# Optimization experiments

Measured on AMD Instinct MI355X. Metric: run time of the kernel, lower is better.

The kernel has to match this reference:

```python
import jax, jax.numpy as jnp
import numpy as np

HEAD_DIM = 64
HIDDEN_SIZE = 3072
NUM_HEADS = 48
B, TXT, VID = 1, 256, 1792
N = TXT + VID


def _layernorm(x, g, b, eps=1e-5):
    mu = jnp.mean(x, axis=-1, keepdims=True)
    xc = x - mu
    var = jnp.mean(xc * xc, axis=-1, keepdims=True)
    return xc * jax.lax.rsqrt(var + eps) * g + b


def _apply_rope1(x, freqs):
    # x: [B, L, H, D]; freqs: [1, 1, Lf, D//2, 2, 2]
    Bx, L, H, D = x.shape
    x_ = x.reshape(Bx, L, H, D // 2, 1, 2)
    # faithful to torch: if dim-2 sizes mismatch (H vs Lf), slice freqs to H
    if x_.shape[2] != 1 and freqs.shape[2] != 1 and x_.shape[2] != freqs.shape[2]:
        freqs = freqs[:, :, : x_.shape[2]]
    out = freqs[..., 0] * x_[..., 0] + freqs[..., 1] * x_[..., 1]
    return out.reshape(Bx, L, H, D).astype(x.dtype)


def setup_inputs() -> dict:
    key = jax.random.key(0)
    ks = jax.random.split(key, 16)
    s = 1.0 / np.sqrt(HIDDEN_SIZE)
    d = dict(
        combined=jax.random.normal(ks[0], (B, N, HIDDEN_SIZE), jnp.float32),
        freqs=jax.random.normal(ks[1], (1, 1, VID, HEAD_DIM // 2, 2, 2), jnp.float32),
        Wq=jax.random.normal(ks[2], (HIDDEN_SIZE, HIDDEN_SIZE), jnp.float32) * s,
        bq=jnp.zeros((HIDDEN_SIZE,), jnp.float32),
        Wk=jax.random.normal(ks[3], (HIDDEN_SIZE, HIDDEN_SIZE), jnp.float32) * s,
        bk=jnp.zeros((HIDDEN_SIZE,), jnp.float32),
        Wv=jax.random.normal(ks[4], (HIDDEN_SIZE, HIDDEN_SIZE), jnp.float32) * s,
        bv=jnp.zeros((HIDDEN_SIZE,), jnp.float32),
        Wo=jax.random.normal(ks[5], (HIDDEN_SIZE, HIDDEN_SIZE), jnp.float32) * s,
        bo=jnp.zeros((HIDDEN_SIZE,), jnp.float32),
        gq=jnp.ones((HEAD_DIM,), jnp.float32),
        bgq=jnp.zeros((HEAD_DIM,), jnp.float32),
        gk=jnp.ones((HEAD_DIM,), jnp.float32),
        bgk=jnp.zeros((HEAD_DIM,), jnp.float32),
        txt_len=TXT,
    )
    return d


def reference(combined, freqs, Wq, bq, Wk, bk, Wv, bv, Wo, bo, gq, bgq, gk, bgk, txt_len):
    Bx, Nx, _ = combined.shape
    Q = (combined @ Wq.T + bq).reshape(Bx, Nx, NUM_HEADS, HEAD_DIM)
    K = (combined @ Wk.T + bk).reshape(Bx, Nx, NUM_HEADS, HEAD_DIM)
    V = (combined @ Wv.T + bv).reshape(Bx, Nx, NUM_HEADS, HEAD_DIM)
    Q = _layernorm(Q, gq, bgq)
    K = _layernorm(K, gk, bgk)
    if freqs is not None and Nx - txt_len > 0:
        Q_vid = _apply_rope1(Q[:, txt_len:], freqs)
        K_vid = _apply_rope1(K[:, txt_len:], freqs)
        Q = jnp.concatenate([Q[:, :txt_len], Q_vid], axis=1)
        K = jnp.concatenate([K[:, :txt_len], K_vid], axis=1)
    # SDPA in fp32: [B, H, N, D]
    q = Q.transpose(0, 2, 1, 3).astype(jnp.float32)
    k = K.transpose(0, 2, 1, 3).astype(jnp.float32)
    v = V.transpose(0, 2, 1, 3).astype(jnp.float32)
    scale = 1.0 / np.sqrt(HEAD_DIM)
    scores = jnp.einsum('bhqd,bhkd->bhqk', q, k) * scale
    probs = jax.nn.softmax(scores, axis=-1)
    attn = jnp.einsum('bhqk,bhkd->bhqd', probs, v).astype(combined.dtype)
    attn = attn.transpose(0, 2, 1, 3).reshape(Bx, Nx, HIDDEN_SIZE)
    out = attn @ Wo.T + bo
    return out[:, txt_len:], out[:, :txt_len]
```

## Files before the change

### kernel.cpp

```cpp
#include <hip/hip_runtime.h>
#include <hip/hip_bf16.h>

typedef __attribute__((ext_vector_type(8))) short bf16x8;
typedef __attribute__((ext_vector_type(4))) float f32x4;
typedef unsigned int __attribute__((address_space(1))) as1_uint;
typedef unsigned int __attribute__((address_space(3))) as3_uint;

#define TXT 256
#define VIDN 1792
#define SEQ 2048
#define HID 3072
#define NH 48
#define HD 64
#define QSCALE 0.18033688011112042f

__device__ __forceinline__ unsigned short f2bf(float f) {
  union { float f; unsigned int u; } x; x.f = f;
  unsigned int r = x.u + 0x7fffu + ((x.u >> 16) & 1u);
  return (unsigned short)(r >> 16);
}

__device__ __forceinline__ void gload16(const void* g, void* l) {
  __builtin_amdgcn_global_load_lds((const as1_uint*)g, (as3_uint*)l, 16, 0, 0);
}

__device__ __forceinline__ void fbar() {
  asm volatile("" ::: "memory");
  __builtin_amdgcn_s_barrier();
  asm volatile("" ::: "memory");
}

__global__ __launch_bounds__(256) void cvt_kernel(const float* __restrict__ s,
                                                  unsigned short* __restrict__ d, int n) {
  int i = (blockIdx.x * 256 + threadIdx.x) * 4;
  if (i >= n) return;
  float4 v = *(const float4*)(s + i);
  ushort4 o;
  o.x = f2bf(v.x); o.y = f2bf(v.y); o.z = f2bf(v.z); o.w = f2bf(v.w);
  *(ushort4*)(d + i) = o;
}

__global__ __launch_bounds__(256) void cvt3_kernel(const float* __restrict__ a,
                                                   const float* __restrict__ b,
                                                   const float* __restrict__ c,
                                                   unsigned short* __restrict__ d) {
  const int per = (HID * HID) / 1024;
  int bid = blockIdx.x;
  int m = bid / per, r = bid - m * per;
  const float* s = (m == 0) ? a : (m == 1) ? b : c;
  int i = (r * 256 + threadIdx.x) * 4;
  float4 v = *(const float4*)(s + i);
  ushort4 o;
  o.x = f2bf(v.x); o.y = f2bf(v.y); o.z = f2bf(v.z); o.w = f2bf(v.w);
  *(ushort4*)(d + (size_t)m * HID * HID + i) = o;
}

template<int MODE>
__global__ __launch_bounds__(512, 4) void gemm256(
    const unsigned short* __restrict__ A,
    const unsigned short* __restrict__ Bt,
    int K, int ntn,
    float* __restrict__ Cq, unsigned short* __restrict__ Vt, const float* __restrict__ bv,
    float* __restrict__ Cout, const float* __restrict__ bo)
{
  __shared__ unsigned short lds[3 * 8192];
  const int tid = threadIdx.x;
  const int mt = blockIdx.x / ntn, nt = blockIdx.x % ntn;
  const int m0 = mt * 128, n0 = nt * 128;
  const int w = tid >> 6, lane = tid & 63, lr = lane & 15, lg = lane >> 4;
  const int wr = w >> 2, wc = w & 3;
  f32x4 acc[4][2] = {};
  const int NT = K >> 5;

  const int soff  = tid * 16;
  const int soffs = soff ^ (((soff >> 7) & 3) << 4);
  const int srow  = soffs >> 6;
  const int scol  = (soffs & 63) >> 1;
  const unsigned short* Asrc = A + (size_t)(m0 + srow) * K + scol;
  const unsigned short* Bsrc = Bt + (size_t)(n0 + srow) * K + scol;

  int aoff[4], boff[2];
#pragma unroll
  for (int mf = 0; mf < 4; ++mf) {
    int arow = wr * 64 + mf * 16 + lr;
    aoff[mf] = arow * 32 + (lg ^ ((arow >> 1) & 3)) * 8;
  }
#pragma unroll
  for (int nf = 0; nf < 2; ++nf) {
    int brow = wc * 32 + nf * 16 + lr;
    boff[nf] = brow * 32 + (lg ^ ((brow >> 1) & 3)) * 8;
  }

#define STAGE(t)                                                               \
  {                                                                            \
    const int slot_ = (t) % 3;                                                 \
    const int k0_ = (t) << 5;                                                  \
    char* base_ = (char*)lds + slot_ * 16384;                                  \
    gload16(Asrc + k0_, base_ + soff);                                         \
    gload16(Bsrc + k0_, base_ + 8192 + soff);                                  \
  }

#define COMPUTE(t)                                                             \
  {                                                                            \
    const unsigned short* lA = lds + ((t) % 3) * 8192;                         \
    const unsigned short* lB = lA + 4096;                                      \
    bf16x8 bfr[2];                                                             \
    _Pragma("unroll")                                                          \
    for (int nf = 0; nf < 2; ++nf)                                             \
      bfr[nf] = *(const bf16x8*)&lB[boff[nf]];                                 \
    __builtin_amdgcn_s_setprio(1);                                             \
    _Pragma("unroll")                                                          \
    for (int mf = 0; mf < 4; ++mf) {                                           \
      bf16x8 af = *(const bf16x8*)&lA[aoff[mf]];                               \
      acc[mf][0] = __builtin_amdgcn_mfma_f32_16x16x32_bf16(af, bfr[0], acc[mf][0], 0, 0, 0); \
      acc[mf][1] = __builtin_amdgcn_mfma_f32_16x16x32_bf16(af, bfr[1], acc[mf][1], 0, 0, 0); \
    }                                                                          \
    __builtin_amdgcn_s_setprio(0);                                             \
  }

  STAGE(0); STAGE(1);
  int t = 0;
  for (; t < NT - 2; ++t) {
    STAGE(t + 2);
    asm volatile("s_waitcnt vmcnt(4)" ::: "memory");
    fbar();
    COMPUTE(t);
    fbar();
  }
  asm volatile("s_waitcnt vmcnt(2)" ::: "memory");
  fbar();
  COMPUTE(t); ++t;
  fbar();
  asm volatile("s_waitcnt vmcnt(0)" ::: "memory");
  fbar();
  COMPUTE(t);
#undef STAGE
#undef COMPUTE

  if (MODE == 0) {
    if (n0 < 6144) {
#pragma unroll
      for (int mf = 0; mf < 4; ++mf) {
        int row = m0 + wr * 64 + mf * 16 + lg * 4;
#pragma unroll
        for (int nf = 0; nf < 2; ++nf) {
          int col = n0 + wc * 32 + nf * 16 + lr;
#pragma unroll
          for (int j = 0; j < 4; ++j)
            Cq[(size_t)(row + j) * 6144 + col] = acc[mf][nf][j];
        }
      }
    } else {
#pragma unroll
      for (int mf = 0; mf < 4; ++mf) {
        int srow2 = m0 + wr * 64 + mf * 16 + lg * 4;
#pragma unroll
        for (int nf = 0; nf < 2; ++nf) {
          int n2 = n0 - 6144 + wc * 32 + nf * 16 + lr;
          float b = bv[n2];
          ushort4 pk;
          pk.x = f2bf(acc[mf][nf][0] + b);
          pk.y = f2bf(acc[mf][nf][1] + b);
          pk.z = f2bf(acc[mf][nf][2] + b);
          pk.w = f2bf(acc[mf][nf][3] + b);
          *(ushort4*)(Vt + (size_t)n2 * SEQ + srow2) = pk;
        }
      }
    }
  } else {
#pragma unroll
    for (int mf = 0; mf < 4; ++mf) {
      int row = m0 + wr * 64 + mf * 16 + lg * 4;
#pragma unroll
      for (int nf = 0; nf < 2; ++nf) {
        int col = n0 + wc * 32 + nf * 16 + lr;
        float b = bo[col];
#pragma unroll
        for (int j = 0; j < 4; ++j) {
          int s = row + j;
          int orow = (s >= TXT) ? (s - TXT) : (VIDN + s);
          Cout[(size_t)orow * HID + col] = acc[mf][nf][j] + b;
        }
      }
    }
  }
}

__global__ __launch_bounds__(256) void ln_rope_kernel(
    const float* __restrict__ QK,
    const float* __restrict__ bq, const float* __restrict__ bk,
    const float* __restrict__ gq, const float* __restrict__ bgq,
    const float* __restrict__ gk, const float* __restrict__ bgk,
    const float* __restrict__ freqs,
    unsigned short* __restrict__ Qh, unsigned short* __restrict__ Kh)
{
  int wid = blockIdx.x * 4 + (threadIdx.x >> 6);
  int lane = threadIdx.x & 63;
  int s = wid / 96;
  int rem = wid - s * 96;
  int h = rem >> 1, qk = rem & 1;
  int col = h * 64 + lane;
  float x = QK[(size_t)s * 6144 + qk * 3072 + col] + (qk ? bk[col] : bq[col]);
  float m = x;
#pragma unroll
  for (int msk = 1; msk < 64; msk <<= 1) m += __shfl_xor(m, msk);
  float mu = m * (1.0f / 64.0f);
  float xc = x - mu;
  float v = xc * xc;
#pragma unroll
  for (int msk = 1; msk < 64; msk <<= 1) v += __shfl_xor(v, msk);
  float rstd = rsqrtf(v * (1.0f / 64.0f) + 1e-5f);
  float y = xc * rstd * (qk ? gk[lane] : gq[lane]) + (qk ? bgk[lane] : bgq[lane]);
  if (s >= TXT) {
    float p = __shfl_xor(y, 1);
    float xe = (lane & 1) ? p : y;
    float xo = (lane & 1) ? y : p;
    int base = h * 128 + (lane >> 1) * 4 + (lane & 1) * 2;
    y = freqs[base] * xe + freqs[base + 1] * xo;
  }
  if (!qk) y *= QSCALE;
  (qk ? Kh : Qh)[((size_t)h * SEQ + s) * 64 + lane] = f2bf(y);
}

__global__ __launch_bounds__(512) void fattn_kernel(
    const unsigned short* __restrict__ Qh, const unsigned short* __restrict__ Kh,
    const unsigned short* __restrict__ Vt, unsigned short* __restrict__ ctx)
{
  __shared__ unsigned short kt[2][64][32];
  __shared__ unsigned short vt[2][64][32];
  __shared__ unsigned short pl[8][16][72];
  const int h = blockIdx.x >> 4;
  const int q0 = (blockIdx.x & 15) * 128;
  const int tid = threadIdx.x, w = tid >> 6, lane = tid & 63, lr = lane & 15, lg = lane >> 4;

  bf16x8 qf0, qf1;
  {
    const unsigned short* qp = Qh + ((size_t)h * SEQ + q0 + w * 16 + lr) * 64 + lg * 8;
    qf0 = *(const bf16x8*)qp;
    qf1 = *(const bf16x8*)(qp + 32);
  }
  f32x4 oacc[4] = {};
  float mrun = -1e30f, lrun = 0.f;

  for (int kv0 = 0; kv0 < SEQ; kv0 += 64) {
    __syncthreads();
    {
      int off = tid * 16;
      int half = off >> 12;
      int rem = off & 4095;
      int row = rem >> 6, cb = rem & 63;
      gload16(Kh + ((size_t)h * SEQ + kv0 + row) * 64 + half * 32 + (cb >> 1), (char*)kt + off);
      gload16(Vt + ((size_t)(h * 64 + row)) * SEQ + kv0 + half * 32 + (cb >> 1), (char*)vt + off);
    }
    __syncthreads();

    f32x4 sacc[4] = {};
    __builtin_amdgcn_s_setprio(1);
#pragma unroll
    for (int nf = 0; nf < 4; ++nf) {
      bf16x8 a0 = *(const bf16x8*)&kt[0][nf * 16 + lr][lg * 8];
      bf16x8 a1 = *(const bf16x8*)&kt[1][nf * 16 + lr][lg * 8];
      sacc[nf] = __builtin_amdgcn_mfma_f32_16x16x32_bf16(a0, qf0, sacc[nf], 0, 0, 0);
      sacc[nf] = __builtin_amdgcn_mfma_f32_16x16x32_bf16(a1, qf1, sacc[nf], 0, 0, 0);
    }
    __builtin_amdgcn_s_setprio(0);

    float mx;
    {
      float t0 = fmaxf(fmaxf(sacc[0][0], sacc[0][1]), fmaxf(sacc[0][2], sacc[0][3]));
      float t1 = fmaxf(fmaxf(sacc[1][0], sacc[1][1]), fmaxf(sacc[1][2], sacc[1][3]));
      float t2 = fmaxf(fmaxf(sacc[2][0], sacc[2][1]), fmaxf(sacc[2][2], sacc[2][3]));
      float t3 = fmaxf(fmaxf(sacc[3][0], sacc[3][1]), fmaxf(sacc[3][2], sacc[3][3]));
      mx = fmaxf(fmaxf(t0, t1), fmaxf(t2, t3));
    }
    mx = fmaxf(mx, __shfl_xor(mx, 16));
    mx = fmaxf(mx, __shfl_xor(mx, 32));

    if (!__all(mx <= mrun + 8.0f)) {
      float mn = fmaxf(mrun, mx);
      float corr = exp2f(mrun - mn);
      lrun *= corr;
      mrun = mn;
      float c0 = __shfl(corr, lg * 4 + 0);
      float c1 = __shfl(corr, lg * 4 + 1);
      float c2 = __shfl(corr, lg * 4 + 2);
      float c3 = __shfl(corr, lg * 4 + 3);
#pragma unroll
      for (int df = 0; df < 4; ++df) {
        oacc[df][0] *= c0; oacc[df][1] *= c1;
        oacc[df][2] *= c2; oacc[df][3] *= c3;
      }
    }

    float pr[4][4];
#pragma unroll
    for (int nf = 0; nf < 4; ++nf)
#pragma unroll
      for (int r = 0; r < 4; ++r)
        pr[nf][r] = exp2f(sacc[nf][r] - mrun);
    float rs;
    {
      float s0 = (pr[0][0] + pr[0][1]) + (pr[0][2] + pr[0][3]);
      float s1 = (pr[1][0] + pr[1][1]) + (pr[1][2] + pr[1][3]);
      float s2 = (pr[2][0] + pr[2][1]) + (pr[2][2] + pr[2][3]);
      float s3 = (pr[3][0] + pr[3][1]) + (pr[3][2] + pr[3][3]);
      rs = (s0 + s1) + (s2 + s3);
    }
    rs += __shfl_xor(rs, 16);
    rs += __shfl_xor(rs, 32);
    lrun += rs;

#pragma unroll
    for (int nf = 0; nf < 4; ++nf) {
      union { __hip_bfloat162 h; unsigned int u; } c0, c1;
      c0.h = __float22bfloat162_rn(make_float2(pr[nf][0], pr[nf][1]));
      c1.h = __float22bfloat162_rn(make_float2(pr[nf][2], pr[nf][3]));
      uint2 pw; pw.x = c0.u; pw.y = c1.u;
      *(uint2*)&pl[w][lr][nf * 16 + lg * 4] = pw;
    }

    bf16x8 pa0 = *(const bf16x8*)&pl[w][lr][lg * 8];
    bf16x8 pa1 = *(const bf16x8*)&pl[w][lr][32 + lg * 8];
    __builtin_amdgcn_s_setprio(1);
#pragma unroll
    for (int df = 0; df < 4; ++df) {
      bf16x8 v0 = *(const bf16x8*)&vt[0][df * 16 + lr][lg * 8];
      bf16x8 v1 = *(const bf16x8*)&vt[1][df * 16 + lr][lg * 8];
      oacc[df] = __builtin_amdgcn_mfma_f32_16x16x32_bf16(pa0, v0, oacc[df], 0, 0, 0);
      oacc[df] = __builtin_amdgcn_mfma_f32_16x16x32_bf16(pa1, v1, oacc[df], 0, 0, 0);
    }
    __builtin_amdgcn_s_setprio(0);
  }

  float linv = 1.0f / lrun;
  float i0 = __shfl(linv, lg * 4 + 0);
  float i1 = __shfl(linv, lg * 4 + 1);
  float i2 = __shfl(linv, lg * 4 + 2);
  float i3 = __shfl(linv, lg * 4 + 3);
#pragma unroll
  for (int df = 0; df < 4; ++df) {
    int s = q0 + w * 16 + lg * 4;
    int dcol = h * 64 + df * 16 + lr;
    ctx[(size_t)(s + 0) * HID + dcol] = f2bf(oacc[df][0] * i0);
    ctx[(size_t)(s + 1) * HID + dcol] = f2bf(oacc[df][1] * i1);
    ctx[(size_t)(s + 2) * HID + dcol] = f2bf(oacc[df][2] * i2);
    ctx[(size_t)(s + 3) * HID + dcol] = f2bf(oacc[df][3] * i3);
  }
}

extern "C" void kernel_launch(void* const* d_in, const int* in_sizes, int n_in,
                              void* d_out, int out_size, void* d_ws, size_t ws_size,
                              hipStream_t stream) {
  const float* combined = (const float*)d_in[0];
  const float* freqs    = (const float*)d_in[1];
  const float* Wq  = (const float*)d_in[2];
  const float* bq  = (const float*)d_in[3];
  const float* Wk  = (const float*)d_in[4];
  const float* bk  = (const float*)d_in[5];
  const float* Wv  = (const float*)d_in[6];
  const float* bv  = (const float*)d_in[7];
  const float* Wo  = (const float*)d_in[8];
  const float* bo  = (const float*)d_in[9];
  const float* gq  = (const float*)d_in[10];
  const float* bgq = (const float*)d_in[11];
  const float* gk  = (const float*)d_in[12];
  const float* bgk = (const float*)d_in[13];
  float* out = (float*)d_out;

  char* ws = (char*)d_ws;
  unsigned short* Abf  = (unsigned short*)ws; ws += (size_t)SEQ * HID * 2;
  unsigned short* Wqkv = (unsigned short*)ws; ws += (size_t)3 * HID * HID * 2;
  float*          QK   = (float*)ws;          ws += (size_t)SEQ * 6144 * 4;
  unsigned short* Qh   = (unsigned short*)ws; ws += (size_t)NH * SEQ * HD * 2;
  unsigned short* Kh   = (unsigned short*)ws; ws += (size_t)NH * SEQ * HD * 2;
  unsigned short* Vt   = (unsigned short*)ws; ws += (size_t)NH * HD * SEQ * 2;
  unsigned short* Wob  = (unsigned short*)QK;
  unsigned short* ctx  = Abf;

  cvt_kernel<<<(SEQ * HID) / 1024, 256, 0, stream>>>(combined, Abf, SEQ * HID);
  cvt3_kernel<<<3 * (HID * HID) / 1024, 256, 0, stream>>>(Wq, Wk, Wv, Wqkv);

  gemm256<0><<<16 * 72, 512, 0, stream>>>(Abf, Wqkv, HID, 72, QK, Vt, bv, nullptr, nullptr);

  ln_rope_kernel<<<(SEQ * NH * 2) / 4, 256, 0, stream>>>(QK, bq, bk, gq, bgq, gk, bgk, freqs, Qh, Kh);

  cvt_kernel<<<(HID * HID) / 1024, 256, 0, stream>>>(Wo, Wob, HID * HID);

  fattn_kernel<<<NH * 16, 512, 0, stream>>>(Qh, Kh, Vt, ctx);

  gemm256<1><<<16 * 24, 512, 0, stream>>>(ctx, Wob, HID, 24, nullptr, nullptr, nullptr, out, bo);
}
```

Baseline: 417.6 us.

## Use 4-wave GEMM with 64x64 warp tiles and double-buffer attention KV loads

```diff
diff --git a/kernel.cpp b/kernel.cpp
--- a/kernel.cpp
+++ b/kernel.cpp
@@ -56,7 +56,7 @@
 }
 
 template<int MODE>
-__global__ __launch_bounds__(512, 4) void gemm256(
+__global__ __launch_bounds__(256, 4) void gemm256(
     const unsigned short* __restrict__ A,
     const unsigned short* __restrict__ Bt,
     int K, int ntn,
@@ -68,26 +68,32 @@
   const int mt = blockIdx.x / ntn, nt = blockIdx.x % ntn;
   const int m0 = mt * 128, n0 = nt * 128;
   const int w = tid >> 6, lane = tid & 63, lr = lane & 15, lg = lane >> 4;
-  const int wr = w >> 2, wc = w & 3;
-  f32x4 acc[4][2] = {};
+  const int wr = w >> 1, wc = w & 1;
+  f32x4 acc[4][4] = {};
   const int NT = K >> 5;
 
-  const int soff  = tid * 16;
-  const int soffs = soff ^ (((soff >> 7) & 3) << 4);
-  const int srow  = soffs >> 6;
-  const int scol  = (soffs & 63) >> 1;
-  const unsigned short* Asrc = A + (size_t)(m0 + srow) * K + scol;
-  const unsigned short* Bsrc = Bt + (size_t)(n0 + srow) * K + scol;
-
-  int aoff[4], boff[2];
+  const unsigned short* Asrc[2];
+  const unsigned short* Bsrc[2];
+  int soffl[2];
+#pragma unroll
+  for (int c = 0; c < 2; ++c) {
+    int so = (c * 256 + tid) * 16;
+    soffl[c] = so;
+    int ss = so ^ (((so >> 7) & 3) << 4);
+    int sr = ss >> 6, sc = (ss & 63) >> 1;
+    Asrc[c] = A + (size_t)(m0 + sr) * K + sc;
+    Bsrc[c] = Bt + (size_t)(n0 + sr) * K + sc;
+  }
+
+  int aoff[4], boff[4];
 #pragma unroll
   for (int mf = 0; mf < 4; ++mf) {
     int arow = wr * 64 + mf * 16 + lr;
     aoff[mf] = arow * 32 + (lg ^ ((arow >> 1) & 3)) * 8;
   }
 #pragma unroll
-  for (int nf = 0; nf < 2; ++nf) {
-    int brow = wc * 32 + nf * 16 + lr;
+  for (int nf = 0; nf < 4; ++nf) {
+    int brow = wc * 64 + nf * 16 + lr;
     boff[nf] = brow * 32 + (lg ^ ((brow >> 1) & 3)) * 8;
   }
 
@@ -96,17 +102,20 @@
     const int slot_ = (t) % 3;                                                 \
     const int k0_ = (t) << 5;                                                  \
     char* base_ = (char*)lds + slot_ * 16384;                                  \
-    gload16(Asrc + k0_, base_ + soff);                                         \
-    gload16(Bsrc + k0_, base_ + 8192 + soff);                                  \
+    _Pragma("unroll")                                                          \
+    for (int c = 0; c < 2; ++c) {                                              \
+      gload16(Asrc[c] + k0_, base_ + soffl[c]);                                \
+      gload16(Bsrc[c] + k0_, base_ + 8192 + soffl[c]);                         \
+    }                                                                          \
   }
 
 #define COMPUTE(t)                                                             \
   {                                                                            \
     const unsigned short* lA = lds + ((t) % 3) * 8192;                         \
     const unsigned short* lB = lA + 4096;                                      \
-    bf16x8 bfr[2];                                                             \
+    bf16x8 bfr[4];                                                             \
     _Pragma("unroll")                                                          \
-    for (int nf = 0; nf < 2; ++nf)                                             \
+    for (int nf = 0; nf < 4; ++nf)                                             \
       bfr[nf] = *(const bf16x8*)&lB[boff[nf]];                                 \
     __builtin_amdgcn_s_setprio(1);                                             \
     _Pragma("unroll")                                                          \
@@ -114,6 +123,8 @@
       bf16x8 af = *(const bf16x8*)&lA[aoff[mf]];                               \
       acc[mf][0] = __builtin_amdgcn_mfma_f32_16x16x32_bf16(af, bfr[0], acc[mf][0], 0, 0, 0); \
       acc[mf][1] = __builtin_amdgcn_mfma_f32_16x16x32_bf16(af, bfr[1], acc[mf][1], 0, 0, 0); \
+      acc[mf][2] = __builtin_amdgcn_mfma_f32_16x16x32_bf16(af, bfr[2], acc[mf][2], 0, 0, 0); \
+      acc[mf][3] = __builtin_amdgcn_mfma_f32_16x16x32_bf16(af, bfr[3], acc[mf][3], 0, 0, 0); \
     }                                                                          \
     __builtin_amdgcn_s_setprio(0);                                             \
   }
@@ -122,12 +133,12 @@
   int t = 0;
   for (; t < NT - 2; ++t) {
     STAGE(t + 2);
-    asm volatile("s_waitcnt vmcnt(4)" ::: "memory");
+    asm volatile("s_waitcnt vmcnt(8)" ::: "memory");
     fbar();
     COMPUTE(t);
     fbar();
   }
-  asm volatile("s_waitcnt vmcnt(2)" ::: "memory");
+  asm volatile("s_waitcnt vmcnt(4)" ::: "memory");
   fbar();
   COMPUTE(t); ++t;
   fbar();
@@ -143,8 +154,8 @@
       for (int mf = 0; mf < 4; ++mf) {
         int row = m0 + wr * 64 + mf * 16 + lg * 4;
 #pragma unroll
-        for (int nf = 0; nf < 2; ++nf) {
-          int col = n0 + wc * 32 + nf * 16 + lr;
+        for (int nf = 0; nf < 4; ++nf) {
+          int col = n0 + wc * 64 + nf * 16 + lr;
 #pragma unroll
           for (int j = 0; j < 4; ++j)
             Cq[(size_t)(row + j) * 6144 + col] = acc[mf][nf][j];
@@ -155,8 +166,8 @@
       for (int mf = 0; mf < 4; ++mf) {
         int srow2 = m0 + wr * 64 + mf * 16 + lg * 4;
 #pragma unroll
-        for (int nf = 0; nf < 2; ++nf) {
-          int n2 = n0 - 6144 + wc * 32 + nf * 16 + lr;
+        for (int nf = 0; nf < 4; ++nf) {
+          int n2 = n0 - 6144 + wc * 64 + nf * 16 + lr;
           float b = bv[n2];
           ushort4 pk;
           pk.x = f2bf(acc[mf][nf][0] + b);
@@ -172,8 +183,8 @@
     for (int mf = 0; mf < 4; ++mf) {
       int row = m0 + wr * 64 + mf * 16 + lg * 4;
 #pragma unroll
-      for (int nf = 0; nf < 2; ++nf) {
-        int col = n0 + wc * 32 + nf * 16 + lr;
+      for (int nf = 0; nf < 4; ++nf) {
+        int col = n0 + wc * 64 + nf * 16 + lr;
         float b = bo[col];
 #pragma unroll
         for (int j = 0; j < 4; ++j) {
@@ -226,8 +237,8 @@
     const unsigned short* __restrict__ Qh, const unsigned short* __restrict__ Kh,
     const unsigned short* __restrict__ Vt, unsigned short* __restrict__ ctx)
 {
-  __shared__ unsigned short kt[2][64][32];
-  __shared__ unsigned short vt[2][64][32];
+  __shared__ unsigned short kt[2][2][64][32];
+  __shared__ unsigned short vt[2][2][64][32];
   __shared__ unsigned short pl[8][16][72];
   const int h = blockIdx.x >> 4;
   const int q0 = (blockIdx.x & 15) * 128;
@@ -242,24 +253,38 @@
   f32x4 oacc[4] = {};
   float mrun = -1e30f, lrun = 0.f;
 
-  for (int kv0 = 0; kv0 < SEQ; kv0 += 64) {
-    __syncthreads();
-    {
-      int off = tid * 16;
-      int half = off >> 12;
-      int rem = off & 4095;
-      int row = rem >> 6, cb = rem & 63;
-      gload16(Kh + ((size_t)h * SEQ + kv0 + row) * 64 + half * 32 + (cb >> 1), (char*)kt + off);
-      gload16(Vt + ((size_t)(h * 64 + row)) * SEQ + kv0 + half * 32 + (cb >> 1), (char*)vt + off);
-    }
-    __syncthreads();
+  const int soff = tid * 16;
+  const int shalf = soff >> 12;
+  const int srem = soff & 4095;
+  const int srow = srem >> 6, scb = srem & 63;
+  const unsigned short* Ksrc = Kh + ((size_t)h * SEQ + srow) * 64 + shalf * 32 + (scb >> 1);
+  const unsigned short* Vsrc = Vt + ((size_t)(h * 64 + srow)) * SEQ + shalf * 32 + (scb >> 1);
+
+#define FSTAGE(t)                                                              \
+  {                                                                            \
+    const int sl_ = (t) & 1;                                                   \
+    const int kv0_ = (t) << 6;                                                 \
+    gload16(Ksrc + (size_t)kv0_ * 64, (char*)kt + sl_ * 8192 + soff);          \
+    gload16(Vsrc + kv0_, (char*)vt + sl_ * 8192 + soff);                       \
+  }
+
+  FSTAGE(0);
+  for (int t = 0; t < 32; ++t) {
+    const int sl = t & 1;
+    if (t < 31) {
+      FSTAGE(t + 1);
+      asm volatile("s_waitcnt vmcnt(2)" ::: "memory");
+    } else {
+      asm volatile("s_waitcnt vmcnt(0)" ::: "memory");
+    }
+    fbar();
 
     f32x4 sacc[4] = {};
     __builtin_amdgcn_s_setprio(1);
 #pragma unroll
     for (int nf = 0; nf < 4; ++nf) {
-      bf16x8 a0 = *(const bf16x8*)&kt[0][nf * 16 + lr][lg * 8];
-      bf16x8 a1 = *(const bf16x8*)&kt[1][nf * 16 + lr][lg * 8];
+      bf16x8 a0 = *(const bf16x8*)&kt[sl][0][nf * 16 + lr][lg * 8];
+      bf16x8 a1 = *(const bf16x8*)&kt[sl][1][nf * 16 + lr][lg * 8];
       sacc[nf] = __builtin_amdgcn_mfma_f32_16x16x32_bf16(a0, qf0, sacc[nf], 0, 0, 0);
       sacc[nf] = __builtin_amdgcn_mfma_f32_16x16x32_bf16(a1, qf1, sacc[nf], 0, 0, 0);
     }
@@ -324,13 +349,16 @@
     __builtin_amdgcn_s_setprio(1);
 #pragma unroll
     for (int df = 0; df < 4; ++df) {
-      bf16x8 v0 = *(const bf16x8*)&vt[0][df * 16 + lr][lg * 8];
-      bf16x8 v1 = *(const bf16x8*)&vt[1][df * 16 + lr][lg * 8];
+      bf16x8 v0 = *(const bf16x8*)&vt[sl][0][df * 16 + lr][lg * 8];
+      bf16x8 v1 = *(const bf16x8*)&vt[sl][1][df * 16 + lr][lg * 8];
       oacc[df] = __builtin_amdgcn_mfma_f32_16x16x32_bf16(pa0, v0, oacc[df], 0, 0, 0);
       oacc[df] = __builtin_amdgcn_mfma_f32_16x16x32_bf16(pa1, v1, oacc[df], 0, 0, 0);
     }
     __builtin_amdgcn_s_setprio(0);
-  }
+
+    fbar();
+  }
+#undef FSTAGE
 
   float linv = 1.0f / lrun;
   float i0 = __shfl(linv, lg * 4 + 0);
@@ -380,7 +408,7 @@
   cvt_kernel<<<(SEQ * HID) / 1024, 256, 0, stream>>>(combined, Abf, SEQ * HID);
   cvt3_kernel<<<3 * (HID * HID) / 1024, 256, 0, stream>>>(Wq, Wk, Wv, Wqkv);
 
-  gemm256<0><<<16 * 72, 512, 0, stream>>>(Abf, Wqkv, HID, 72, QK, Vt, bv, nullptr, nullptr);
+  gemm256<0><<<16 * 72, 256, 0, stream>>>(Abf, Wqkv, HID, 72, QK, Vt, bv, nullptr, nullptr);
 
   ln_rope_kernel<<<(SEQ * NH * 2) / 4, 256, 0, stream>>>(QK, bq, bk, gq, bgq, gk, bgk, freqs, Qh, Kh);
 
@@ -388,5 +416,5 @@
 
   fattn_kernel<<<NH * 16, 512, 0, stream>>>(Qh, Kh, Vt, ctx);
 
-  gemm256<1><<<16 * 24, 512, 0, stream>>>(ctx, Wob, HID, 24, nullptr, nullptr, nullptr, out, bo);
-}
+  gemm256<1><<<16 * 24, 256, 0, stream>>>(ctx, Wob, HID, 24, nullptr, nullptr, nullptr, out, bo);
+}
```

New measurement: 404.2 us. 1.03x faster.

## Double-buffer K/V tiles in flash attention and merge input conversion kernels

Applied to the files above, without the earlier changes.

```diff
diff --git a/kernel.cpp b/kernel.cpp
--- a/kernel.cpp
+++ b/kernel.cpp
@@ -40,19 +40,25 @@
   *(ushort4*)(d + i) = o;
 }
 
-__global__ __launch_bounds__(256) void cvt3_kernel(const float* __restrict__ a,
-                                                   const float* __restrict__ b,
-                                                   const float* __restrict__ c,
-                                                   unsigned short* __restrict__ d) {
-  const int per = (HID * HID) / 1024;
+__global__ __launch_bounds__(256) void cvt4_kernel(
+    const float* __restrict__ comb, const float* __restrict__ wq,
+    const float* __restrict__ wk, const float* __restrict__ wv,
+    unsigned short* __restrict__ abf, unsigned short* __restrict__ wqkv) {
+  const int CB = (SEQ * HID) / 1024;
+  const int WB = (HID * HID) / 1024;
   int bid = blockIdx.x;
-  int m = bid / per, r = bid - m * per;
-  const float* s = (m == 0) ? a : (m == 1) ? b : c;
+  const float* s; unsigned short* d; int r;
+  if (bid < CB) { s = comb; d = abf; r = bid; }
+  else {
+    int q = bid - CB; int m = q / WB; r = q - m * WB;
+    s = (m == 0) ? wq : (m == 1) ? wk : wv;
+    d = wqkv + (size_t)m * HID * HID;
+  }
   int i = (r * 256 + threadIdx.x) * 4;
   float4 v = *(const float4*)(s + i);
   ushort4 o;
   o.x = f2bf(v.x); o.y = f2bf(v.y); o.z = f2bf(v.z); o.w = f2bf(v.w);
-  *(ushort4*)(d + (size_t)m * HID * HID + i) = o;
+  *(ushort4*)(d + i) = o;
 }
 
 template<int MODE>
@@ -226,8 +232,8 @@
     const unsigned short* __restrict__ Qh, const unsigned short* __restrict__ Kh,
     const unsigned short* __restrict__ Vt, unsigned short* __restrict__ ctx)
 {
-  __shared__ unsigned short kt[2][64][32];
-  __shared__ unsigned short vt[2][64][32];
+  __shared__ unsigned short kt[2][2][64][32];
+  __shared__ unsigned short vt[2][2][64][32];
   __shared__ unsigned short pl[8][16][72];
   const int h = blockIdx.x >> 4;
   const int q0 = (blockIdx.x & 15) * 128;
@@ -242,24 +248,38 @@
   f32x4 oacc[4] = {};
   float mrun = -1e30f, lrun = 0.f;
 
-  for (int kv0 = 0; kv0 < SEQ; kv0 += 64) {
-    __syncthreads();
-    {
-      int off = tid * 16;
-      int half = off >> 12;
-      int rem = off & 4095;
-      int row = rem >> 6, cb = rem & 63;
-      gload16(Kh + ((size_t)h * SEQ + kv0 + row) * 64 + half * 32 + (cb >> 1), (char*)kt + off);
-      gload16(Vt + ((size_t)(h * 64 + row)) * SEQ + kv0 + half * 32 + (cb >> 1), (char*)vt + off);
-    }
-    __syncthreads();
+  const int soff = tid * 16;
+  const int shalf = soff >> 12;
+  const int srem = soff & 4095;
+  const int srow = srem >> 6, scb = srem & 63;
+  const unsigned short* Ksrc = Kh + ((size_t)h * SEQ + srow) * 64 + shalf * 32 + (scb >> 1);
+  const unsigned short* Vsrc = Vt + ((size_t)(h * 64 + srow)) * SEQ + shalf * 32 + (scb >> 1);
+
+#define FSTAGE(t)                                                              \
+  {                                                                            \
+    const int sl_ = (t) & 1;                                                   \
+    const int kv0_ = (t) << 6;                                                 \
+    gload16(Ksrc + (size_t)kv0_ * 64, (char*)kt + sl_ * 8192 + soff);          \
+    gload16(Vsrc + kv0_, (char*)vt + sl_ * 8192 + soff);                       \
+  }
+
+  FSTAGE(0);
+  for (int t = 0; t < 32; ++t) {
+    const int sl = t & 1;
+    if (t < 31) {
+      FSTAGE(t + 1);
+      asm volatile("s_waitcnt vmcnt(2)" ::: "memory");
+    } else {
+      asm volatile("s_waitcnt vmcnt(0)" ::: "memory");
+    }
+    fbar();
 
     f32x4 sacc[4] = {};
     __builtin_amdgcn_s_setprio(1);
 #pragma unroll
     for (int nf = 0; nf < 4; ++nf) {
-      bf16x8 a0 = *(const bf16x8*)&kt[0][nf * 16 + lr][lg * 8];
-      bf16x8 a1 = *(const bf16x8*)&kt[1][nf * 16 + lr][lg * 8];
+      bf16x8 a0 = *(const bf16x8*)&kt[sl][0][nf * 16 + lr][lg * 8];
+      bf16x8 a1 = *(const bf16x8*)&kt[sl][1][nf * 16 + lr][lg * 8];
       sacc[nf] = __builtin_amdgcn_mfma_f32_16x16x32_bf16(a0, qf0, sacc[nf], 0, 0, 0);
       sacc[nf] = __builtin_amdgcn_mfma_f32_16x16x32_bf16(a1, qf1, sacc[nf], 0, 0, 0);
     }
@@ -324,13 +344,16 @@
     __builtin_amdgcn_s_setprio(1);
 #pragma unroll
     for (int df = 0; df < 4; ++df) {
-      bf16x8 v0 = *(const bf16x8*)&vt[0][df * 16 + lr][lg * 8];
-      bf16x8 v1 = *(const bf16x8*)&vt[1][df * 16 + lr][lg * 8];
+      bf16x8 v0 = *(const bf16x8*)&vt[sl][0][df * 16 + lr][lg * 8];
+      bf16x8 v1 = *(const bf16x8*)&vt[sl][1][df * 16 + lr][lg * 8];
       oacc[df] = __builtin_amdgcn_mfma_f32_16x16x32_bf16(pa0, v0, oacc[df], 0, 0, 0);
       oacc[df] = __builtin_amdgcn_mfma_f32_16x16x32_bf16(pa1, v1, oacc[df], 0, 0, 0);
     }
     __builtin_amdgcn_s_setprio(0);
-  }
+
+    fbar();
+  }
+#undef FSTAGE
 
   float linv = 1.0f / lrun;
   float i0 = __shfl(linv, lg * 4 + 0);
@@ -377,8 +400,8 @@
   unsigned short* Wob  = (unsigned short*)QK;
   unsigned short* ctx  = Abf;
 
-  cvt_kernel<<<(SEQ * HID) / 1024, 256, 0, stream>>>(combined, Abf, SEQ * HID);
-  cvt3_kernel<<<3 * (HID * HID) / 1024, 256, 0, stream>>>(Wq, Wk, Wv, Wqkv);
+  cvt4_kernel<<<(SEQ * HID) / 1024 + 3 * (HID * HID) / 1024, 256, 0, stream>>>(
+      combined, Wq, Wk, Wv, Abf, Wqkv);
 
   gemm256<0><<<16 * 72, 512, 0, stream>>>(Abf, Wqkv, HID, 72, QK, Vt, bv, nullptr, nullptr);
 
```

Measured after the change: 405.7 us. 2.8% less time.
